# Kernel optimization log

Measured on AMD Instinct MI355X. Metric: run time of the kernel, lower is better.

The kernel has to match this reference:

```python
import jax, jax.numpy as jnp
import numpy as np

K = 4096          # num_embeddings
D = 256           # embedding_dim
BETA = 0.25
DECAY = 0.99
EPS = 1e-05

def setup_inputs() -> dict:
    key = jax.random.key(0)
    k1, k2, k3 = jax.random.split(key, 3)
    N = 65536
    return {
        "z": jax.random.normal(k1, (N, D), dtype=jnp.float32),
        "weight": jax.random.normal(k2, (K, D), dtype=jnp.float32),
        "ema_w": jax.random.normal(k3, (K, D), dtype=jnp.float32),
        "ema_cluster_size": jnp.ones((K,), dtype=jnp.float32),
    }

def reference(z, weight, ema_w, ema_cluster_size):
    # pairwise squared distances: [N, K]
    d = (jnp.sum(z * z, axis=1, keepdims=True)
         + jnp.sum(weight * weight, axis=1)
         - 2.0 * jnp.matmul(z, weight.T))
    idx = jnp.argmin(d, axis=1)                     # [N]
    encodings = jax.nn.one_hot(idx, K, dtype=z.dtype)  # [N, K]

    # EMA codebook update (training branch). In torch the results are re-wrapped
    # into fresh nn.Parameters, which detaches them from the autograd graph.
    def _ema(z_, enc_, ema_w_, cs_):
        cs = cs_ * DECAY + (1.0 - DECAY) * jnp.sum(enc_, axis=0)
        n = jnp.sum(cs)
        cs = (cs + EPS) / (n + K * EPS) * n
        dw = jnp.matmul(enc_.T, z_)                 # [K, D] scatter-add of z by code
        new_ema_w = ema_w_ * DECAY + (1.0 - DECAY) * dw
        new_weight = new_ema_w / cs[:, None]
        return cs, new_ema_w, new_weight
    new_cs, new_ema_w, new_weight = jax.lax.stop_gradient(
        _ema(z, encodings, ema_w, ema_cluster_size))

    z_q = new_weight[idx]                           # [N, D] gather from updated codebook
    loss = (jnp.mean((jax.lax.stop_gradient(z_q) - z) ** 2)
            + BETA * jnp.mean((z_q - jax.lax.stop_gradient(z)) ** 2))
    avg_probs = jnp.mean(encodings, axis=0)
    perplexity = jnp.exp(-jnp.sum(avg_probs * jnp.log(avg_probs + 1e-10)))
    z_q = z + jax.lax.stop_gradient(z_q - z)        # straight-through estimator
    return (z_q, idx[:, None], loss, perplexity, new_cs, new_ema_w, new_weight)
```

## Files before the change

### kernel.cpp

```cpp
#include <hip/hip_runtime.h>
#include <math.h>

#define NPTS 65536
#define DIMD 256
#define KCB  4096
#define MARGIN 2.0f

#define O_ZQ   0
#define O_IDX  16777216
#define O_LOSS 16842752
#define O_PERP 16842753
#define O_CS   16842754
#define O_EMAW 16846850
#define O_W    17895426

#define OFF_WSW   8388608
#define OFF_CCNT  8912896
#define OFF_CIDS  8978432
#define OFF_OFFS  10027008
#define OFF_CUR   10031232
#define OFF_ROWS  10035328
#define OFF_GMIN  10100864
#define OFF_CHOF  10166400

#define CHK 64
#define MAXCHUNKS 5120

typedef __attribute__((ext_vector_type(8))) short short8;
typedef __attribute__((ext_vector_type(4))) float f32x4;

__device__ __forceinline__ unsigned short f2bf(float f) {
    unsigned u = __float_as_uint(f);
    return (unsigned short)((u + 0x7FFF + ((u >> 16) & 1)) >> 16);
}
__device__ __forceinline__ unsigned encf(float f) {
    unsigned u = __float_as_uint(f);
    return (u >> 31) ? ~u : (u | 0x80000000u);
}
__device__ __forceinline__ float decf(unsigned e) {
    unsigned u = (e & 0x80000000u) ? (e & 0x7fffffffu) : ~e;
    return __uint_as_float(u);
}

__global__ void k_prepz(const float* __restrict__ src, unsigned* __restrict__ dst,
                        float* __restrict__ ss) {
    int l   = threadIdx.x & 63;
    int row = blockIdx.x * 4 + (threadIdx.x >> 6);
    float4 v = ((const float4*)(src + (size_t)row * DIMD))[l];
    uint2 pk = make_uint2(f2bf(v.x) | (f2bf(v.y) << 16),
                          f2bf(v.z) | (f2bf(v.w) << 16));
    ((uint2*)dst)[(size_t)row * 64 + l] = pk;
    float s = v.x*v.x + v.y*v.y + v.z*v.z + v.w*v.w;
    #pragma unroll
    for (int off = 32; off; off >>= 1) s += __shfl_down(s, off);
    if (l == 0) ss[row] = s;
}

__global__ void k_prepw(const float* __restrict__ src, unsigned* __restrict__ dst,
                        float* __restrict__ ss) {
    int l   = threadIdx.x & 63;
    int row = blockIdx.x * 4 + (threadIdx.x >> 6);
    float4 v = ((const float4*)(src + (size_t)row * DIMD))[l];
    uint2 pk = make_uint2(f2bf(v.x) | (f2bf(v.y) << 16),
                          f2bf(v.z) | (f2bf(v.w) << 16));
    int g = row >> 4, n16 = row & 15;
    int c = l >> 3, q = (l >> 1) & 3, half = l & 1;
    ((uint2*)dst)[g * 1024 + c * 128 + (q * 16 + n16) * 2 + half] = pk;
    float s = v.x*v.x + v.y*v.y + v.z*v.z + v.w*v.w;
    #pragma unroll
    for (int off = 32; off; off >>= 1) s += __shfl_down(s, off);
    if (l == 0) ss[row] = s;
}

#define BUFG 4
#define NBUF 32

__launch_bounds__(256, 2)
__global__ void k_pass0(const unsigned* __restrict__ zbf,
                        const uint4* __restrict__ wsw4,
                        const float* __restrict__ wwg,
                        unsigned* __restrict__ gmin) {
    __shared__ __align__(16) char smem[2][BUFG * 8192];
    const int t = threadIdx.x, wv = t >> 6, l = t & 63;
    const int q = l >> 4, n16 = l & 15;
    const int rb    = blockIdx.x >> 1;
    const int half  = blockIdx.x & 1;
    const int row0  = rb * 256 + wv * 64;
    const int g0    = half * 128;
    const int phase = (blockIdx.x * 7) & 31;

    union U { uint4 u; short8 s; } afr[4][8];
    #pragma unroll
    for (int s = 0; s < 4; ++s) {
        const char* zb = (const char*)zbf + ((size_t)(row0 + s * 16 + n16) << 9) + q * 16;
        #pragma unroll
        for (int c = 0; c < 8; ++c) afr[s][c].u = *(const uint4*)(zb + c * 64);
    }

    auto stage = [&](int which, int bi) {
        const uint4* srcb = wsw4 + (size_t)(g0 + ((phase + bi) & 31) * BUFG) * 512;
        #pragma unroll
        for (int j = 0; j < 8; ++j) {
            int rrow = j * 4 + wv;
            __builtin_amdgcn_global_load_lds(
                (const __attribute__((address_space(1))) unsigned*)(srcb + rrow * 64 + l),
                (__attribute__((address_space(3))) unsigned*)(&smem[which][rrow * 1024]),
                16, 0, 0);
        }
    };

    float minv[16];
    #pragma unroll
    for (int i = 0; i < 16; ++i) minv[i] = 3.0e38f;

    stage(0, 0);
    __syncthreads();

    for (int b = 0; b < NBUF; ++b) {
        const int cur = b & 1;
        if (b + 1 < NBUF) stage(cur ^ 1, b + 1);
        const char* sbase = smem[cur];
        const int ggb = g0 + ((phase + b) & 31) * BUFG;
        #pragma unroll
        for (int g2 = 0; g2 < BUFG; ++g2) {
            f32x4 acc[4];
            #pragma unroll
            for (int s = 0; s < 4; ++s) acc[s] = (f32x4){0.f, 0.f, 0.f, 0.f};
            #pragma unroll
            for (int c = 0; c < 8; ++c) {
                U bf; bf.u = *(const uint4*)(sbase + g2 * 8192 + c * 1024 + (l << 4));
                #pragma unroll
                for (int s = 0; s < 4; ++s)
                    acc[s] = __builtin_amdgcn_mfma_f32_16x16x32_bf16(afr[s][c].s, bf.s, acc[s], 0, 0, 0);
            }
            float wwv = wwg[(ggb + g2) * 16 + n16];
            #pragma unroll
            for (int s = 0; s < 4; ++s)
                #pragma unroll
                for (int r = 0; r < 4; ++r)
                    minv[s*4+r] = fminf(minv[s*4+r], fmaf(-2.f, acc[s][r], wwv));
        }
        __syncthreads();
    }

    #pragma unroll
    for (int i = 0; i < 16; ++i) {
        float m = minv[i];
        #pragma unroll
        for (int msk = 1; msk < 16; msk <<= 1) m = fminf(m, __shfl_xor(m, msk));
        if (n16 == 0)
            atomicMin(&gmin[row0 + (i >> 2) * 16 + q * 4 + (i & 3)], encf(m));
    }
}

__launch_bounds__(256, 2)
__global__ void k_pass1(const unsigned* __restrict__ zbf,
                        const uint4* __restrict__ wsw4,
                        const float* __restrict__ wwg,
                        const unsigned* __restrict__ gmin,
                        int* __restrict__ ccnt,
                        int* __restrict__ cids) {
    __shared__ __align__(16) char smem[2][BUFG * 8192];
    const int t = threadIdx.x, wv = t >> 6, l = t & 63;
    const int q = l >> 4, n16 = l & 15;
    const int rb    = blockIdx.x >> 1;
    const int half  = blockIdx.x & 1;
    const int row0  = rb * 256 + wv * 64;
    const int g0    = half * 128;
    const int phase = (blockIdx.x * 7) & 31;

    union U { uint4 u; short8 s; } afr[4][8];
    #pragma unroll
    for (int s = 0; s < 4; ++s) {
        const char* zb = (const char*)zbf + ((size_t)(row0 + s * 16 + n16) << 9) + q * 16;
        #pragma unroll
        for (int c = 0; c < 8; ++c) afr[s][c].u = *(const uint4*)(zb + c * 64);
    }

    auto stage = [&](int which, int bi) {
        const uint4* srcb = wsw4 + (size_t)(g0 + ((phase + bi) & 31) * BUFG) * 512;
        #pragma unroll
        for (int j = 0; j < 8; ++j) {
            int rrow = j * 4 + wv;
            __builtin_amdgcn_global_load_lds(
                (const __attribute__((address_space(1))) unsigned*)(srcb + rrow * 64 + l),
                (__attribute__((address_space(3))) unsigned*)(&smem[which][rrow * 1024]),
                16, 0, 0);
        }
    };

    float thr[16];
    #pragma unroll
    for (int i = 0; i < 16; ++i)
        thr[i] = decf(gmin[row0 + (i >> 2) * 16 + q * 4 + (i & 3)]) + MARGIN;

    stage(0, 0);
    __syncthreads();

    for (int b = 0; b < NBUF; ++b) {
        const int cur = b & 1;
        if (b + 1 < NBUF) stage(cur ^ 1, b + 1);
        const char* sbase = smem[cur];
        const int ggb = g0 + ((phase + b) & 31) * BUFG;
        #pragma unroll
        for (int g2 = 0; g2 < BUFG; ++g2) {
            f32x4 acc[4];
            #pragma unroll
            for (int s = 0; s < 4; ++s) acc[s] = (f32x4){0.f, 0.f, 0.f, 0.f};
            #pragma unroll
            for (int c = 0; c < 8; ++c) {
                U bf; bf.u = *(const uint4*)(sbase + g2 * 8192 + c * 1024 + (l << 4));
                #pragma unroll
                for (int s = 0; s < 4; ++s)
                    acc[s] = __builtin_amdgcn_mfma_f32_16x16x32_bf16(afr[s][c].s, bf.s, acc[s], 0, 0, 0);
            }
            const int gg = ggb + g2;
            float wwv = wwg[gg * 16 + n16];
            #pragma unroll
            for (int s = 0; s < 4; ++s)
                #pragma unroll
                for (int r = 0; r < 4; ++r) {
                    float core = fmaf(-2.f, acc[s][r], wwv);
                    if (core <= thr[s*4+r]) {
                        int row = row0 + s * 16 + q * 4 + r;
                        int pos = atomicAdd(&ccnt[row], 1);
                        if (pos < 16) cids[row * 16 + pos] = gg * 16 + n16;
                    }
                }
        }
        __syncthreads();
    }
}

__global__ void k_refine(const float* __restrict__ z,
                         const float* __restrict__ w,
                         const float* __restrict__ zz,
                         const float* __restrict__ wwg,
                         const int* __restrict__ ccnt,
                         const int* __restrict__ cids,
                         float* __restrict__ counts,
                         int*   __restrict__ idxi,
                         float* __restrict__ idxf) {
    int l   = threadIdx.x & 63;
    int row = blockIdx.x * 4 + (threadIdx.x >> 6);
    int n = ccnt[row]; if (n > 16) n = 16;
    float4 zv = ((const float4*)(z + (size_t)row * DIMD))[l];
    float zzv = zz[row];
    float bd = 3.0e38f; int bi = 0x7fffffff;
    for (int j = 0; j < n; ++j) {
        int k = cids[row * 16 + j];
        float4 wv = ((const float4*)(w + (size_t)k * DIMD))[l];
        float s = zv.x*wv.x + zv.y*wv.y + zv.z*wv.z + zv.w*wv.w;
        #pragma unroll
        for (int off = 32; off; off >>= 1) s += __shfl_xor(s, off);
        float d = (zzv + wwg[k]) - 2.0f * s;
        if (d < bd || (d == bd && k < bi)) { bd = d; bi = k; }
    }
    if (l == 0) {
        idxi[row] = bi;
        idxf[row] = (float)bi;
        atomicAdd(&counts[bi], 1.0f);
    }
}

__global__ void k_offsets(const float* __restrict__ counts,
                          int* __restrict__ offs, int* __restrict__ cursor,
                          int* __restrict__ choffs) {
    __shared__ int sc[1024];
    int t = threadIdx.x;
    int c[4]; int s = 0;
    #pragma unroll
    for (int i = 0; i < 4; ++i) { c[i] = (int)counts[t * 4 + i]; s += c[i]; }
    sc[t] = s;
    __syncthreads();
    for (int d = 1; d < 1024; d <<= 1) {
        int v = (t >= d) ? sc[t - d] : 0;
        __syncthreads();
        sc[t] += v;
        __syncthreads();
    }
    int o = sc[t] - s;
    #pragma unroll
    for (int i = 0; i < 4; ++i) { offs[t*4+i] = o; cursor[t*4+i] = o; o += c[i]; }
    if (t == 1023) offs[4096] = sc[1023];
    __syncthreads();

    int ch[4]; int s2 = 0;
    #pragma unroll
    for (int i = 0; i < 4; ++i) { ch[i] = (c[i] + CHK - 1) / CHK; s2 += ch[i]; }
    sc[t] = s2;
    __syncthreads();
    for (int d = 1; d < 1024; d <<= 1) {
        int v = (t >= d) ? sc[t - d] : 0;
        __syncthreads();
        sc[t] += v;
        __syncthreads();
    }
    int o2 = sc[t] - s2;
    #pragma unroll
    for (int i = 0; i < 4; ++i) { choffs[t*4+i] = o2; o2 += ch[i]; }
    if (t == 1023) choffs[4096] = sc[1023];
}

__global__ void k_fill(const int* __restrict__ idxi, int* __restrict__ cursor,
                       int* __restrict__ rows) {
    int r = blockIdx.x * 256 + threadIdx.x;
    int k = idxi[r];
    int pos = atomicAdd(&cursor[k], 1);
    rows[pos] = r;
}

__global__ void k_dw(const float* __restrict__ z, const int* __restrict__ offs,
                     const int* __restrict__ choffs, const int* __restrict__ rows,
                     float* __restrict__ dw) {
    __shared__ float4 part[4][64];
    int b = blockIdx.x;
    if (b >= choffs[KCB]) return;
    int lo = 0, hi = KCB;
    while (hi - lo > 1) { int mid = (lo + hi) >> 1; if (choffs[mid] <= b) lo = mid; else hi = mid; }
    int k  = lo;
    int ci = b - choffs[k];
    int o0 = offs[k] + ci * CHK;
    int o1 = offs[k + 1]; if (o1 > o0 + CHK) o1 = o0 + CHK;
    int l = threadIdx.x & 63, j = threadIdx.x >> 6;
    float4 a = make_float4(0.f, 0.f, 0.f, 0.f);
    for (int i = o0 + j; i < o1; i += 4) {
        int r = rows[i];
        float4 v = ((const float4*)(z + (size_t)r * DIMD))[l];
        a.x += v.x; a.y += v.y; a.z += v.z; a.w += v.w;
    }
    part[j][l] = a;
    __syncthreads();
    if (j == 0) {
        float4 bb = part[0][l], c = part[1][l], d = part[2][l], e = part[3][l];
        a = make_float4(bb.x+c.x+d.x+e.x, bb.y+c.y+d.y+e.y,
                        bb.z+c.z+d.z+e.z, bb.w+c.w+d.w+e.w);
        float* p = dw + (size_t)k * DIMD + l * 4;
        if (choffs[k + 1] - choffs[k] == 1) {
            *(float4*)p = a;
        } else {
            atomicAdd(p + 0, a.x); atomicAdd(p + 1, a.y);
            atomicAdd(p + 2, a.z); atomicAdd(p + 3, a.w);
        }
    }
}

__global__ void k_cs(const float* __restrict__ ema_cs,
                     float* __restrict__ cs_io,
                     float* __restrict__ perp) {
    __shared__ float2 red[16];
    int t = threadIdx.x;
    float csd[4];
    float nl = 0.f, el = 0.f;
    #pragma unroll
    for (int i = 0; i < 4; ++i) {
        int k = t * 4 + i;
        float c  = cs_io[k];
        float cd = ema_cs[k] * 0.99f + 0.01f * c;
        csd[i] = cd;
        nl += cd;
        float p = c * (1.0f / 65536.0f);
        el += p * logf(p + 1e-10f);
    }
    #pragma unroll
    for (int off = 32; off; off >>= 1) { nl += __shfl_down(nl, off); el += __shfl_down(el, off); }
    if ((t & 63) == 0) red[t >> 6] = make_float2(nl, el);
    __syncthreads();
    if (t == 0) {
        float n = 0.f, e = 0.f;
        for (int i = 0; i < 16; ++i) { n += red[i].x; e += red[i].y; }
        red[0] = make_float2(n, e);
        perp[0] = expf(-e);
    }
    __syncthreads();
    float n = red[0].x;
    float scale = n / (n + 4096.0f * 1e-5f);
    #pragma unroll
    for (int i = 0; i < 4; ++i)
        cs_io[t * 4 + i] = (csd[i] + 1e-5f) * scale;
}

__global__ void k_emaw(const float* __restrict__ ema_w,
                       const float* __restrict__ cs,
                       float* __restrict__ emaw_io,
                       float* __restrict__ wout) {
    int i = (blockIdx.x * 256 + threadIdx.x) * 4;
    int k = i >> 8;
    float4 dv = *(const float4*)(emaw_io + i);
    float4 ev = *(const float4*)(ema_w + i);
    float c = cs[k];
    float4 ne;
    ne.x = ev.x * 0.99f + 0.01f * dv.x;
    ne.y = ev.y * 0.99f + 0.01f * dv.y;
    ne.z = ev.z * 0.99f + 0.01f * dv.z;
    ne.w = ev.w * 0.99f + 0.01f * dv.w;
    *(float4*)(emaw_io + i) = ne;
    float4 nw = make_float4(ne.x / c, ne.y / c, ne.z / c, ne.w / c);
    *(float4*)(wout + i) = nw;
}

__global__ void k_zq(const float* __restrict__ z,
                     const float* __restrict__ wnew,
                     const int* __restrict__ idxi,
                     float* __restrict__ zq,
                     float* __restrict__ sqacc) {
    __shared__ float red[4];
    int i = (blockIdx.x * 256 + threadIdx.x) * 4;
    int n = i >> 8;
    int d = i & 255;
    int k = idxi[n];
    float4 wv = *(const float4*)(wnew + (k << 8) + d);
    float4 zv = *(const float4*)(z + i);
    float4 o;
    o.x = zv.x + (wv.x - zv.x);
    o.y = zv.y + (wv.y - zv.y);
    o.z = zv.z + (wv.z - zv.z);
    o.w = zv.w + (wv.w - zv.w);
    *(float4*)(zq + i) = o;
    float dx = wv.x - zv.x, dy = wv.y - zv.y, dz = wv.z - zv.z, dw_ = wv.w - zv.w;
    float s = dx*dx + dy*dy + dz*dz + dw_*dw_;
    #pragma unroll
    for (int off = 32; off; off >>= 1) s += __shfl_down(s, off);
    int lane = threadIdx.x & 63;
    if (lane == 0) red[threadIdx.x >> 6] = s;
    __syncthreads();
    if (threadIdx.x == 0)
        atomicAdd(&sqacc[blockIdx.x & 255], red[0] + red[1] + red[2] + red[3]);
}

__global__ void k_final(const float* __restrict__ sqacc, float* __restrict__ loss) {
    __shared__ float red[4];
    int t = threadIdx.x;
    float s = sqacc[t];
    #pragma unroll
    for (int off = 32; off; off >>= 1) s += __shfl_down(s, off);
    if ((t & 63) == 0) red[t >> 6] = s;
    __syncthreads();
    if (t == 0)
        loss[0] = 1.25f * (red[0] + red[1] + red[2] + red[3]) * (1.0f / 16777216.0f);
}

extern "C" void kernel_launch(void* const* d_in, const int* in_sizes, int n_in,
                              void* d_out, int out_size, void* d_ws, size_t ws_size,
                              hipStream_t stream) {
    const float* z      = (const float*)d_in[0];
    const float* weight = (const float*)d_in[1];
    const float* ema_w  = (const float*)d_in[2];
    const float* ema_cs = (const float*)d_in[3];
    float* out = (float*)d_out;
    float* ws  = (float*)d_ws;

    float* scal = ws + 4096;
    int*   idxi = (int*)(ws + 8192);

    unsigned* zbf    = (unsigned*)(out + O_ZQ);
    uint4*    wsw4   = (uint4*)(out + O_ZQ + OFF_WSW);
    int*      ccnt   = (int*)(out + O_ZQ + OFF_CCNT);
    int*      cids   = (int*)(out + O_ZQ + OFF_CIDS);
    int*      offs   = (int*)(out + O_ZQ + OFF_OFFS);
    int*      cursor = (int*)(out + O_ZQ + OFF_CUR);
    int*      rows   = (int*)(out + O_ZQ + OFF_ROWS);
    unsigned* gmin   = (unsigned*)(out + O_ZQ + OFF_GMIN);
    int*      choffs = (int*)(out + O_ZQ + OFF_CHOF);
    float*    zz     = out + O_EMAW;
    float*    wwg    = out + O_EMAW + 65536;

    hipMemsetAsync(scal,       0,    256 * 4, stream);
    hipMemsetAsync(out + O_CS, 0,    (size_t)KCB * 4, stream);
    hipMemsetAsync(ccnt,       0,    (size_t)NPTS * 4, stream);
    hipMemsetAsync(gmin,       0xFF, (size_t)NPTS * 4, stream);

    k_prepz  <<<NPTS / 4, 256, 0, stream>>>(z, zbf, zz);
    k_prepw  <<<KCB  / 4, 256, 0, stream>>>(weight, (unsigned*)wsw4, wwg);
    k_pass0  <<<512, 256, 0, stream>>>(zbf, wsw4, wwg, gmin);
    k_pass1  <<<512, 256, 0, stream>>>(zbf, wsw4, wwg, gmin, ccnt, cids);
    k_refine <<<NPTS / 4, 256, 0, stream>>>(z, weight, zz, wwg, ccnt, cids,
                                            out + O_CS, idxi, out + O_IDX);
    hipMemsetAsync(out + O_EMAW, 0, (size_t)KCB * DIMD * 4, stream);
    k_offsets<<<1, 1024, 0, stream>>>(out + O_CS, offs, cursor, choffs);
    k_fill   <<<NPTS / 256, 256, 0, stream>>>(idxi, cursor, rows);
    k_cs     <<<1, 1024, 0, stream>>>(ema_cs, out + O_CS, out + O_PERP);
    k_dw     <<<MAXCHUNKS, 256, 0, stream>>>(z, offs, choffs, rows, out + O_EMAW);
    k_emaw   <<<(KCB * DIMD) / 1024, 256, 0, stream>>>(ema_w, out + O_CS,
                                                       out + O_EMAW, out + O_W);
    k_zq     <<<(NPTS * DIMD) / 1024, 256, 0, stream>>>(z, out + O_W, idxi,
                                                        out + O_ZQ, scal);
    k_final  <<<1, 256, 0, stream>>>(scal, out + O_LOSS);
}
```

Before: 532.1 us.

## Use 6-slot LDS ring with deeper prefetch and LDS-local candidate collection

Replaces the double-buffered 4-group staging with a 6-slot ring of single-group buffers, prefetch distance 4 and partial vmcnt waits, so each step needs one barrier instead of a full __syncthreads. It caches the codebook norms in LDS, raises wave priority around MFMA blocks, and changes the block phase stagger. In pass1, candidate appends go to LDS counters and lists first and are flushed to global with one atomic per row. This adds LDS usage and more barriers per group, which may reduce occupancy or raise sync overhead.

```diff
diff --git a/kernel.cpp b/kernel.cpp
--- a/kernel.cpp
+++ b/kernel.cpp
@@ -25,6 +25,9 @@
 
 #define CHK 64
 #define MAXCHUNKS 5120
+
+#define RING 6
+#define PFD  4
 
 typedef __attribute__((ext_vector_type(8))) short short8;
 typedef __attribute__((ext_vector_type(4))) float f32x4;
@@ -72,22 +75,20 @@
     if (l == 0) ss[row] = s;
 }
 
-#define BUFG 4
-#define NBUF 32
-
 __launch_bounds__(256, 2)
 __global__ void k_pass0(const unsigned* __restrict__ zbf,
                         const uint4* __restrict__ wsw4,
                         const float* __restrict__ wwg,
                         unsigned* __restrict__ gmin) {
-    __shared__ __align__(16) char smem[2][BUFG * 8192];
+    __shared__ __align__(16) char smem[RING * 8192];
+    __shared__ float lds_ww[2048];
     const int t = threadIdx.x, wv = t >> 6, l = t & 63;
     const int q = l >> 4, n16 = l & 15;
     const int rb    = blockIdx.x >> 1;
     const int half  = blockIdx.x & 1;
     const int row0  = rb * 256 + wv * 64;
     const int g0    = half * 128;
-    const int phase = (blockIdx.x * 7) & 31;
+    const int ph0   = (blockIdx.x * 37) & 127;
 
     union U { uint4 u; short8 s; } afr[4][8];
     #pragma unroll
@@ -97,50 +98,80 @@
         for (int c = 0; c < 8; ++c) afr[s][c].u = *(const uint4*)(zb + c * 64);
     }
 
-    auto stage = [&](int which, int bi) {
-        const uint4* srcb = wsw4 + (size_t)(g0 + ((phase + bi) & 31) * BUFG) * 512;
-        #pragma unroll
-        for (int j = 0; j < 8; ++j) {
+    auto stage = [&](int buf, int g) {
+        const int ga = (ph0 + g) & 127;
+        const uint4* srcb = wsw4 + (size_t)(g0 + ga) * 512;
+        #pragma unroll
+        for (int j = 0; j < 2; ++j) {
             int rrow = j * 4 + wv;
             __builtin_amdgcn_global_load_lds(
                 (const __attribute__((address_space(1))) unsigned*)(srcb + rrow * 64 + l),
-                (__attribute__((address_space(3))) unsigned*)(&smem[which][rrow * 1024]),
+                (__attribute__((address_space(3))) unsigned*)(&smem[buf * 8192 + rrow * 1024]),
                 16, 0, 0);
         }
     };
 
+    for (int i = t; i < 2048; i += 256) lds_ww[i] = wwg[g0 * 16 + i];
+    #pragma unroll
+    for (int g = 0; g < PFD; ++g) stage(g, g);
+    __syncthreads();
+
     float minv[16];
     #pragma unroll
     for (int i = 0; i < 16; ++i) minv[i] = 3.0e38f;
 
-    stage(0, 0);
-    __syncthreads();
-
-    for (int b = 0; b < NBUF; ++b) {
-        const int cur = b & 1;
-        if (b + 1 < NBUF) stage(cur ^ 1, b + 1);
-        const char* sbase = smem[cur];
-        const int ggb = g0 + ((phase + b) & 31) * BUFG;
-        #pragma unroll
-        for (int g2 = 0; g2 < BUFG; ++g2) {
-            f32x4 acc[4];
-            #pragma unroll
-            for (int s = 0; s < 4; ++s) acc[s] = (f32x4){0.f, 0.f, 0.f, 0.f};
-            #pragma unroll
-            for (int c = 0; c < 8; ++c) {
-                U bf; bf.u = *(const uint4*)(sbase + g2 * 8192 + c * 1024 + (l << 4));
-                #pragma unroll
-                for (int s = 0; s < 4; ++s)
-                    acc[s] = __builtin_amdgcn_mfma_f32_16x16x32_bf16(afr[s][c].s, bf.s, acc[s], 0, 0, 0);
-            }
-            float wwv = wwg[(ggb + g2) * 16 + n16];
+    int buf = 0, sbuf = PFD;
+    #pragma unroll 1
+    for (int g = 0; g < 128 - PFD; ++g) {
+        stage(sbuf, g + PFD);
+        sbuf = (sbuf == RING - 1) ? 0 : sbuf + 1;
+        asm volatile("s_waitcnt vmcnt(8)" ::: "memory");
+        __builtin_amdgcn_s_barrier();
+        const char* sbase = smem + buf * 8192;
+        buf = (buf == RING - 1) ? 0 : buf + 1;
+        const int ga = (ph0 + g) & 127;
+        f32x4 acc[4];
+        #pragma unroll
+        for (int s = 0; s < 4; ++s) acc[s] = (f32x4){0.f, 0.f, 0.f, 0.f};
+        __builtin_amdgcn_s_setprio(1);
+        #pragma unroll
+        for (int c = 0; c < 8; ++c) {
+            U bf; bf.u = *(const uint4*)(sbase + c * 1024 + (l << 4));
             #pragma unroll
             for (int s = 0; s < 4; ++s)
-                #pragma unroll
-                for (int r = 0; r < 4; ++r)
-                    minv[s*4+r] = fminf(minv[s*4+r], fmaf(-2.f, acc[s][r], wwv));
-        }
-        __syncthreads();
+                acc[s] = __builtin_amdgcn_mfma_f32_16x16x32_bf16(afr[s][c].s, bf.s, acc[s], 0, 0, 0);
+        }
+        __builtin_amdgcn_s_setprio(0);
+        float wwv = lds_ww[ga * 16 + n16];
+        #pragma unroll
+        for (int s = 0; s < 4; ++s)
+            #pragma unroll
+            for (int r = 0; r < 4; ++r)
+                minv[s*4+r] = fminf(minv[s*4+r], fmaf(-2.f, acc[s][r], wwv));
+    }
+    #pragma unroll 1
+    for (int g = 128 - PFD; g < 128; ++g) {
+        asm volatile("s_waitcnt vmcnt(0)" ::: "memory");
+        __builtin_amdgcn_s_barrier();
+        const char* sbase = smem + buf * 8192;
+        buf = (buf == RING - 1) ? 0 : buf + 1;
+        const int ga = (ph0 + g) & 127;
+        f32x4 acc[4];
+        #pragma unroll
+        for (int s = 0; s < 4; ++s) acc[s] = (f32x4){0.f, 0.f, 0.f, 0.f};
+        #pragma unroll
+        for (int c = 0; c < 8; ++c) {
+            U bf; bf.u = *(const uint4*)(sbase + c * 1024 + (l << 4));
+            #pragma unroll
+            for (int s = 0; s < 4; ++s)
+                acc[s] = __builtin_amdgcn_mfma_f32_16x16x32_bf16(afr[s][c].s, bf.s, acc[s], 0, 0, 0);
+        }
+        float wwv = lds_ww[ga * 16 + n16];
+        #pragma unroll
+        for (int s = 0; s < 4; ++s)
+            #pragma unroll
+            for (int r = 0; r < 4; ++r)
+                minv[s*4+r] = fminf(minv[s*4+r], fmaf(-2.f, acc[s][r], wwv));
     }
 
     #pragma unroll
@@ -160,14 +191,17 @@
                         const unsigned* __restrict__ gmin,
                         int* __restrict__ ccnt,
                         int* __restrict__ cids) {
-    __shared__ __align__(16) char smem[2][BUFG * 8192];
+    __shared__ __align__(16) char smem[RING * 8192];
+    __shared__ float lds_ww[2048];
+    __shared__ int   lds_cnt[256];
+    __shared__ short lds_cid[256 * 16];
     const int t = threadIdx.x, wv = t >> 6, l = t & 63;
     const int q = l >> 4, n16 = l & 15;
     const int rb    = blockIdx.x >> 1;
     const int half  = blockIdx.x & 1;
     const int row0  = rb * 256 + wv * 64;
     const int g0    = half * 128;
-    const int phase = (blockIdx.x * 7) & 31;
+    const int ph0   = (blockIdx.x * 37) & 127;
 
     union U { uint4 u; short8 s; } afr[4][8];
     #pragma unroll
@@ -177,14 +211,15 @@
         for (int c = 0; c < 8; ++c) afr[s][c].u = *(const uint4*)(zb + c * 64);
     }
 
-    auto stage = [&](int which, int bi) {
-        const uint4* srcb = wsw4 + (size_t)(g0 + ((phase + bi) & 31) * BUFG) * 512;
-        #pragma unroll
-        for (int j = 0; j < 8; ++j) {
+    auto stage = [&](int buf, int g) {
+        const int ga = (ph0 + g) & 127;
+        const uint4* srcb = wsw4 + (size_t)(g0 + ga) * 512;
+        #pragma unroll
+        for (int j = 0; j < 2; ++j) {
             int rrow = j * 4 + wv;
             __builtin_amdgcn_global_load_lds(
                 (const __attribute__((address_space(1))) unsigned*)(srcb + rrow * 64 + l),
-                (__attribute__((address_space(3))) unsigned*)(&smem[which][rrow * 1024]),
+                (__attribute__((address_space(3))) unsigned*)(&smem[buf * 8192 + rrow * 1024]),
                 16, 0, 0);
         }
     };
@@ -194,41 +229,63 @@
     for (int i = 0; i < 16; ++i)
         thr[i] = decf(gmin[row0 + (i >> 2) * 16 + q * 4 + (i & 3)]) + MARGIN;
 
-    stage(0, 0);
-    __syncthreads();
-
-    for (int b = 0; b < NBUF; ++b) {
-        const int cur = b & 1;
-        if (b + 1 < NBUF) stage(cur ^ 1, b + 1);
-        const char* sbase = smem[cur];
-        const int ggb = g0 + ((phase + b) & 31) * BUFG;
-        #pragma unroll
-        for (int g2 = 0; g2 < BUFG; ++g2) {
-            f32x4 acc[4];
-            #pragma unroll
-            for (int s = 0; s < 4; ++s) acc[s] = (f32x4){0.f, 0.f, 0.f, 0.f};
-            #pragma unroll
-            for (int c = 0; c < 8; ++c) {
-                U bf; bf.u = *(const uint4*)(sbase + g2 * 8192 + c * 1024 + (l << 4));
-                #pragma unroll
-                for (int s = 0; s < 4; ++s)
-                    acc[s] = __builtin_amdgcn_mfma_f32_16x16x32_bf16(afr[s][c].s, bf.s, acc[s], 0, 0, 0);
-            }
-            const int gg = ggb + g2;
-            float wwv = wwg[gg * 16 + n16];
+    for (int i = t; i < 2048; i += 256) lds_ww[i] = wwg[g0 * 16 + i];
+    lds_cnt[t] = 0;
+    #pragma unroll
+    for (int g = 0; g < PFD; ++g) stage(g, g);
+    __syncthreads();
+
+    int buf = 0, sbuf = PFD;
+    #pragma unroll 1
+    for (int g = 0; g < 128; ++g) {
+        if (g < 128 - PFD) {
+            stage(sbuf, g + PFD);
+            sbuf = (sbuf == RING - 1) ? 0 : sbuf + 1;
+            asm volatile("s_waitcnt vmcnt(8)" ::: "memory");
+        } else {
+            asm volatile("s_waitcnt vmcnt(0)" ::: "memory");
+        }
+        __builtin_amdgcn_s_barrier();
+        const char* sbase = smem + buf * 8192;
+        buf = (buf == RING - 1) ? 0 : buf + 1;
+        const int ga = (ph0 + g) & 127;
+        f32x4 acc[4];
+        #pragma unroll
+        for (int s = 0; s < 4; ++s) acc[s] = (f32x4){0.f, 0.f, 0.f, 0.f};
+        __builtin_amdgcn_s_setprio(1);
+        #pragma unroll
+        for (int c = 0; c < 8; ++c) {
+            U bf; bf.u = *(const uint4*)(sbase + c * 1024 + (l << 4));
             #pragma unroll
             for (int s = 0; s < 4; ++s)
-                #pragma unroll
-                for (int r = 0; r < 4; ++r) {
-                    float core = fmaf(-2.f, acc[s][r], wwv);
-                    if (core <= thr[s*4+r]) {
-                        int row = row0 + s * 16 + q * 4 + r;
-                        int pos = atomicAdd(&ccnt[row], 1);
-                        if (pos < 16) cids[row * 16 + pos] = gg * 16 + n16;
-                    }
+                acc[s] = __builtin_amdgcn_mfma_f32_16x16x32_bf16(afr[s][c].s, bf.s, acc[s], 0, 0, 0);
+        }
+        __builtin_amdgcn_s_setprio(0);
+        const int gg = g0 + ga;
+        float wwv = lds_ww[ga * 16 + n16];
+        #pragma unroll
+        for (int s = 0; s < 4; ++s)
+            #pragma unroll
+            for (int r = 0; r < 4; ++r) {
+                float core = fmaf(-2.f, acc[s][r], wwv);
+                if (core <= thr[s*4+r]) {
+                    int rl = wv * 64 + s * 16 + q * 4 + r;
+                    int p = atomicAdd(&lds_cnt[rl], 1);
+                    if (p < 16) lds_cid[rl * 16 + p] = (short)(gg * 16 + n16);
                 }
-        }
-        __syncthreads();
+            }
+    }
+
+    __syncthreads();
+    int n = lds_cnt[t];
+    if (n > 0) {
+        int rg = rb * 256 + t;
+        int base = atomicAdd(&ccnt[rg], n);
+        int m = n > 16 ? 16 : n;
+        for (int j = 0; j < m; ++j) {
+            int p = base + j;
+            if (p < 16) cids[rg * 16 + p] = (int)lds_cid[t * 16 + j];
+        }
     }
 }
 
```

Result: faster. 513.2 us (-3.5%).
